# Kernel optimization log

Hardware: AMD Instinct MI355X
Metric: run time of the kernel (lower is better)

Reference implementation:

```python
import jax, jax.numpy as jnp
import numpy as np


def setup_inputs() -> dict:
    key = jax.random.key(0)
    k1, k2 = jax.random.split(key)
    z = jax.random.normal(k1, (16, 2048, 512), dtype=jnp.float32)
    embedding = jax.random.normal(k2, (8192, 512), dtype=jnp.float32)
    return {"z": z, "embedding": embedding}


def reference(z, embedding):
    BETA = 0.25
    B, N, D = z.shape
    n_codes = embedding.shape[0]
    flat_z = z.reshape(-1, D)  # [M, D], M = B*N
    # squared euclidean distances: ||z||^2 - 2 z.e^T + ||e||^2 -> [M, n_codes]
    dist = (jnp.sum(flat_z * flat_z, axis=1, keepdims=True)
            - 2.0 * jnp.matmul(flat_z, embedding.T)
            + jnp.sum(embedding * embedding, axis=1))
    codes = jnp.argmin(dist, axis=1)  # [M]
    z_q = embedding[codes].reshape(B, N, D)
    # straight-through estimator
    z_q_st = z + jax.lax.stop_gradient(z_q - z)
    loss = BETA * jnp.mean((z_q_st - jax.lax.stop_gradient(z)) ** 2)
    # codebook usage stats (equivalent to one_hot.mean(0))
    counts = jnp.zeros((n_codes,), dtype=flat_z.dtype).at[codes].add(1.0)
    avg_probs = counts / flat_z.shape[0]
    perp = jnp.exp(-jnp.sum(avg_probs * jnp.log(avg_probs + 1e-10)))
    return z_q_st, codes.reshape(B, N), loss, perp
```

## Files before the change

kernel.cpp:

```cpp
#include <hip/hip_runtime.h>
#include <stdint.h>
#include <stddef.h>

#define M_ROWS 32768
#define N_CODES 8192
#define K_DIM 512
#define BM 128
#define BN 128
#define BK 64
#define KITERS (K_DIM / BK)
#define CAND_CAP (3u*1024u*1024u)
#define LCAP 512u
#define TAU2 2.0f

#define OFF_CODES 16777216
#define OFF_LOSS  (16777216 + 32768)
#define OFF_PERP  (16777216 + 32768 + 1)

using short8  = __attribute__((ext_vector_type(8))) short;
using ushort8 = __attribute__((ext_vector_type(8))) unsigned short;
using f32x4   = __attribute__((ext_vector_type(4))) float;

typedef unsigned short u16;
typedef unsigned int   u32;
typedef unsigned long long u64;

__device__ __forceinline__ u32 ford(float f) {
    u32 u = __float_as_uint(f);
    return (u & 0x80000000u) ? ~u : (u | 0x80000000u);
}
__device__ __forceinline__ float fordinv(u32 u) {
    u32 v = (u & 0x80000000u) ? (u & 0x7FFFFFFFu) : ~u;
    return __uint_as_float(v);
}
__device__ __forceinline__ u16 f2bf(float f) {
    u32 u = __float_as_uint(f);
    u = u + 0x7FFFu + ((u >> 16) & 1u);
    return (u16)(u >> 16);
}

__device__ __forceinline__ void ldg_to_lds16(const u16* g, u16* l) {
    __builtin_amdgcn_global_load_lds((__attribute__((address_space(1))) void*)(g),
                                     (__attribute__((address_space(3))) void*)(l),
                                     16, 0, 0);
}

__global__ void k_init(u32* rowMin, u64* rowBest, u32* counts, u32* candCnt) {
    int i = blockIdx.x * blockDim.x + threadIdx.x;
    if (i < M_ROWS) { rowMin[i] = 0xFFFFFFFFu; rowBest[i] = ~0ull; }
    if (i < N_CODES) counts[i] = 0u;
    if (i == 0) *candCnt = 0u;
}

__global__ void k_convert(const float* __restrict__ src, u16* __restrict__ dst,
                          float* __restrict__ nrm2, int nrows) {
    int row  = blockIdx.x * 4 + (threadIdx.x >> 6);
    int lane = threadIdx.x & 63;
    if (row >= nrows) return;
    const float* p = src + (size_t)row * K_DIM + lane * 8;
    float4 a = *(const float4*)p;
    float4 b = *(const float4*)(p + 4);
    ushort8 v;
    v[0]=f2bf(a.x); v[1]=f2bf(a.y); v[2]=f2bf(a.z); v[3]=f2bf(a.w);
    v[4]=f2bf(b.x); v[5]=f2bf(b.y); v[6]=f2bf(b.z); v[7]=f2bf(b.w);
    *(ushort8*)(dst + (size_t)row * K_DIM + lane * 8) = v;
    float ss = a.x*a.x + a.y*a.y + a.z*a.z + a.w*a.w
             + b.x*b.x + b.y*b.y + b.z*b.z + b.w*b.w;
    #pragma unroll
    for (int s = 32; s; s >>= 1) ss += __shfl_xor(ss, s);
    if (lane == 0) nrm2[row] = ss;
}

__global__ __launch_bounds__(256, 4)
void k_gemm(const u16* __restrict__ zb, const u16* __restrict__ eb,
            const float* __restrict__ en2, u32* __restrict__ rowMin,
            u32* __restrict__ candCnt, u64* __restrict__ cand) {
    __shared__ __align__(16) u16 As[BM * BK];
    __shared__ __align__(16) u16 Bs[BN * BK];
    __shared__ float en2s[BN];
    __shared__ u32 threshL[BM];
    __shared__ u64 candBuf[LCAP];
    __shared__ u32 ldsCnt, ldsBase;

    const int tid  = threadIdx.x;
    const int lane = tid & 63;
    const int wave = tid >> 6;
    const int rowTile = blockIdx.x * BM;
    const int nTile   = blockIdx.y * BN;
    const int wm = (wave >> 1) * 64;
    const int wn = (wave & 1) * 64;

    if (tid < BN) { en2s[tid] = en2[nTile + tid]; threshL[tid] = 0xFFFFFFFFu; }
    if (tid == 0) ldsCnt = 0u;

    const int srow = (lane >> 3);
    const int sg   = (lane & 7) ^ ((lane >> 3) & 7);
    const u16* gA[4]; const u16* gB[4]; u16* lA[4]; u16* lB[4];
    #pragma unroll
    for (int t = 0; t < 4; t++) {
        int i = wave * 4 + t;
        gA[t] = zb + (size_t)(rowTile + i * 8 + srow) * K_DIM + sg * 8;
        gB[t] = eb + (size_t)(nTile   + i * 8 + srow) * K_DIM + sg * 8;
        lA[t] = As + i * 512;
        lB[t] = Bs + i * 512;
    }

    int aoff[4], boff[4];
    const int q = lane >> 4;
    #pragma unroll
    for (int t = 0; t < 4; t++) {
        int R  = wm + t * 16 + (lane & 15);
        aoff[t] = (R * 8 + (q ^ (R & 7))) * 16;
        int Rn = wn + t * 16 + (lane & 15);
        boff[t] = (Rn * 8 + (q ^ (Rn & 7))) * 16;
    }

    f32x4 acc[4][4] = {};

    for (int kk = 0; kk < KITERS; kk++) {
        const int ko = kk * BK;
        #pragma unroll
        for (int t = 0; t < 4; t++) {
            ldg_to_lds16(gA[t] + ko, lA[t]);
            ldg_to_lds16(gB[t] + ko, lB[t]);
        }
        __syncthreads();
        short8 af[4], bf_[4];
        #pragma unroll
        for (int t = 0; t < 4; t++) {
            af[t]  = *(const short8*)((const char*)As + aoff[t]);
            bf_[t] = *(const short8*)((const char*)Bs + boff[t]);
        }
        #pragma unroll
        for (int i = 0; i < 4; i++)
            #pragma unroll
            for (int j = 0; j < 4; j++)
                acc[i][j] = __builtin_amdgcn_mfma_f32_16x16x32_bf16(af[i], bf_[j], acc[i][j], 0, 0, 0);
        #pragma unroll
        for (int t = 0; t < 4; t++) {
            af[t]  = *(const short8*)((const char*)As + (aoff[t] ^ 64));
            bf_[t] = *(const short8*)((const char*)Bs + (boff[t] ^ 64));
        }
        #pragma unroll
        for (int i = 0; i < 4; i++)
            #pragma unroll
            for (int j = 0; j < 4; j++)
                acc[i][j] = __builtin_amdgcn_mfma_f32_16x16x32_bf16(af[i], bf_[j], acc[i][j], 0, 0, 0);
        __syncthreads();
    }

    float e2v[4];
    #pragma unroll
    for (int j = 0; j < 4; j++) e2v[j] = en2s[wn + j * 16 + (lane & 15)];
    #pragma unroll
    for (int i = 0; i < 4; i++)
        #pragma unroll
        for (int j = 0; j < 4; j++)
            #pragma unroll
            for (int r = 0; r < 4; r++)
                acc[i][j][r] = e2v[j] - 2.0f * acc[i][j][r];

    float rm[4][4];
    #pragma unroll
    for (int i = 0; i < 4; i++)
        #pragma unroll
        for (int r = 0; r < 4; r++)
            rm[i][r] = fminf(fminf(acc[i][0][r], acc[i][1][r]),
                             fminf(acc[i][2][r], acc[i][3][r]));
    #pragma unroll
    for (int d = 1; d < 16; d <<= 1)
        #pragma unroll
        for (int i = 0; i < 4; i++)
            #pragma unroll
            for (int r = 0; r < 4; r++)
                rm[i][r] = fminf(rm[i][r], __shfl_xor(rm[i][r], d));

    if ((lane & 15) == 0) {
        #pragma unroll
        for (int i = 0; i < 4; i++)
            #pragma unroll
            for (int r = 0; r < 4; r++) {
                int lrow = wm + i * 16 + (lane >> 4) * 4 + r;
                u32 o = ford(rm[i][r]);
                atomicMin(&threshL[lrow], o);
                u32 old = atomicMin(&rowMin[rowTile + lrow], o);
                atomicMin(&threshL[lrow], old);
            }
    }
    __syncthreads();

    #pragma unroll
    for (int i = 0; i < 4; i++) {
        #pragma unroll
        for (int r = 0; r < 4; r++) {
            int lrow = wm + i * 16 + (lane >> 4) * 4 + r;
            float th = fordinv(threshL[lrow]) + TAU2;
            #pragma unroll
            for (int j = 0; j < 4; j++) {
                float sv = acc[i][j][r];
                if (sv <= th) {
                    u32 code = (u32)(nTile + wn + j * 16 + (lane & 15));
                    u64 pk = ((u64)ford(sv) << 32) |
                             (u64)(((u32)(rowTile + lrow) << 13) | code);
                    u32 idx = atomicAdd(&ldsCnt, 1u);
                    if (idx < LCAP) candBuf[idx] = pk;
                    else { u32 g = atomicAdd(candCnt, 1u);
                           if (g < CAND_CAP) cand[g] = pk; }
                }
            }
        }
    }
    __syncthreads();
    if (tid == 0) {
        u32 n = ldsCnt < LCAP ? ldsCnt : LCAP;
        ldsBase = atomicAdd(candCnt, n);
    }
    __syncthreads();
    u32 n = ldsCnt < LCAP ? ldsCnt : LCAP;
    for (u32 k2 = tid; k2 < n; k2 += 256) {
        u32 g = ldsBase + k2;
        if (g < CAND_CAP) cand[g] = candBuf[k2];
    }
}

__global__ void k_refine(const float* __restrict__ z, const float* __restrict__ emb,
                         const float* __restrict__ en2, const u32* __restrict__ candCnt,
                         const u64* __restrict__ cand, const u32* __restrict__ rowMin,
                         u64* __restrict__ rowBest) {
    u32 cnt = *candCnt; if (cnt > CAND_CAP) cnt = CAND_CAP;
    int gt = blockIdx.x * blockDim.x + threadIdx.x;
    u32 wid = (u32)(gt >> 6);
    int lane = gt & 63;
    u32 nw = (u32)((gridDim.x * blockDim.x) >> 6);
    for (u32 ci = wid; ci < cnt; ci += nw) {
        u64 pk = cand[ci];
        u32 rc = (u32)pk;
        u32 row = rc >> 13, code = rc & (N_CODES - 1);
        float ad = fordinv((u32)(pk >> 32));
        float gm = fordinv(rowMin[row]);
        if (ad > gm + TAU2) continue;
        const float4* zp = (const float4*)(z + (size_t)row * K_DIM) + lane * 2;
        const float4* ep = (const float4*)(emb + (size_t)code * K_DIM) + lane * 2;
        float4 a0 = zp[0], a1 = zp[1], b0 = ep[0], b1 = ep[1];
        float d = a0.x*b0.x + a0.y*b0.y + a0.z*b0.z + a0.w*b0.w
                + a1.x*b1.x + a1.y*b1.y + a1.z*b1.z + a1.w*b1.w;
        #pragma unroll
        for (int s = 32; s; s >>= 1) d += __shfl_xor(d, s);
        if (lane == 0) {
            float sv = en2[code] - 2.0f * d;
            u64 bk = ((u64)ford(sv) << 32) | (u64)code;
            atomicMin(rowBest + row, bk);
        }
    }
}

__global__ void k_output(const u64* __restrict__ rowBest, const float* __restrict__ emb,
                         float* __restrict__ out, u32* __restrict__ counts) {
    int row = blockIdx.x;
    u64 pk = rowBest[row];
    u32 code = (u32)(pk & 0xFFFFFFFFull);
    int t = threadIdx.x;
    float4 v = ((const float4*)(emb + (size_t)code * K_DIM))[t];
    ((float4*)(out + (size_t)row * K_DIM))[t] = v;
    if (t == 0) {
        out[OFF_CODES + row] = (float)code;
        atomicAdd(&counts[code], 1u);
    }
}

__global__ void k_final(const u64* __restrict__ rowBest, const float* __restrict__ zn2,
                        const u32* __restrict__ counts, float* __restrict__ out) {
    __shared__ float red[256];
    int t = threadIdx.x;
    float s1 = 0.f;
    for (int r = t; r < M_ROWS; r += 256)
        s1 += zn2[r] + fordinv((u32)(rowBest[r] >> 32));
    red[t] = s1; __syncthreads();
    for (int w = 128; w; w >>= 1) { if (t < w) red[t] += red[t + w]; __syncthreads(); }
    float lossSum = red[0];
    __syncthreads();
    float s2 = 0.f;
    for (int c = t; c < N_CODES; c += 256) {
        float p = (float)counts[c] * (1.0f / (float)M_ROWS);
        s2 += p * logf(p + 1e-10f);
    }
    red[t] = s2; __syncthreads();
    for (int w = 128; w; w >>= 1) { if (t < w) red[t] += red[t + w]; __syncthreads(); }
    if (t == 0) {
        out[OFF_LOSS] = 0.25f * lossSum / ((float)M_ROWS * (float)K_DIM);
        out[OFF_PERP] = expf(-red[0]);
    }
}

#define WS_ZB      ((size_t)0)
#define WS_EB      ((size_t)33554432)
#define WS_EN2     ((size_t)41943040)
#define WS_ZN2     ((size_t)41975808)
#define WS_ROWMIN  ((size_t)42106880)
#define WS_ROWBEST ((size_t)42237952)
#define WS_COUNTS  ((size_t)42500096)
#define WS_CANDCNT ((size_t)42532864)
#define WS_CAND    ((size_t)42533120)

extern "C" void kernel_launch(void* const* d_in, const int* in_sizes, int n_in,
                              void* d_out, int out_size, void* d_ws, size_t ws_size,
                              hipStream_t stream) {
    const float* z   = (const float*)d_in[0];
    const float* emb = (const float*)d_in[1];
    float* out = (float*)d_out;
    char* ws = (char*)d_ws;

    u16*  zb      = (u16*)(ws + WS_ZB);
    u16*  eb      = (u16*)(ws + WS_EB);
    float* en2    = (float*)(ws + WS_EN2);
    float* zn2    = (float*)(ws + WS_ZN2);
    u32*  rowMin  = (u32*)(ws + WS_ROWMIN);
    u64*  rowBest = (u64*)(ws + WS_ROWBEST);
    u32*  counts  = (u32*)(ws + WS_COUNTS);
    u32*  candCnt = (u32*)(ws + WS_CANDCNT);
    u64*  cand    = (u64*)(ws + WS_CAND);

    k_init<<<dim3(M_ROWS / 256), dim3(256), 0, stream>>>(rowMin, rowBest, counts, candCnt);
    k_convert<<<dim3(M_ROWS / 4), dim3(256), 0, stream>>>(z, zb, zn2, M_ROWS);
    k_convert<<<dim3(N_CODES / 4), dim3(256), 0, stream>>>(emb, eb, en2, N_CODES);
    k_gemm<<<dim3(M_ROWS / BM, N_CODES / BN), dim3(256), 0, stream>>>(zb, eb, en2, rowMin, candCnt, cand);
    k_refine<<<dim3(1024), dim3(256), 0, stream>>>(z, emb, en2, candCnt, cand, rowMin, rowBest);
    k_output<<<dim3(M_ROWS), dim3(128), 0, stream>>>(rowBest, emb, out, counts);
    k_final<<<dim3(1), dim3(256), 0, stream>>>(rowBest, zn2, counts, out);
}
```

Measured before the change: 647.7 us.

## Fuse init into convert, batch refine candidates, widen output and parallelize final

```diff
diff --git a/kernel.cpp b/kernel.cpp
--- a/kernel.cpp
+++ b/kernel.cpp
@@ -45,15 +45,16 @@
                                      16, 0, 0);
 }
 
-__global__ void k_init(u32* rowMin, u64* rowBest, u32* counts, u32* candCnt) {
-    int i = blockIdx.x * blockDim.x + threadIdx.x;
-    if (i < M_ROWS) { rowMin[i] = 0xFFFFFFFFu; rowBest[i] = ~0ull; }
-    if (i < N_CODES) counts[i] = 0u;
-    if (i == 0) *candCnt = 0u;
-}
-
 __global__ void k_convert(const float* __restrict__ src, u16* __restrict__ dst,
-                          float* __restrict__ nrm2, int nrows) {
+                          float* __restrict__ nrm2, int nrows,
+                          u32* rowMin, u64* rowBest, u32* counts, u32* candCnt,
+                          float* fsum, u32* ticket) {
+    if (rowMin) {
+        int g = blockIdx.x * blockDim.x + threadIdx.x;
+        if (g < M_ROWS) { rowMin[g] = 0xFFFFFFFFu; rowBest[g] = ~0ull; }
+        if (g < N_CODES) counts[g] = 0u;
+        if (g == 0) { *candCnt = 0u; *fsum = 0.f; *ticket = 0u; }
+    }
     int row  = blockIdx.x * 4 + (threadIdx.x >> 6);
     int lane = threadIdx.x & 63;
     if (row >= nrows) return;
@@ -232,34 +233,46 @@
     u32 wid = (u32)(gt >> 6);
     int lane = gt & 63;
     u32 nw = (u32)((gridDim.x * blockDim.x) >> 6);
-    for (u32 ci = wid; ci < cnt; ci += nw) {
-        u64 pk = cand[ci];
-        u32 rc = (u32)pk;
-        u32 row = rc >> 13, code = rc & (N_CODES - 1);
-        float ad = fordinv((u32)(pk >> 32));
-        float gm = fordinv(rowMin[row]);
-        if (ad > gm + TAU2) continue;
-        const float4* zp = (const float4*)(z + (size_t)row * K_DIM) + lane * 2;
-        const float4* ep = (const float4*)(emb + (size_t)code * K_DIM) + lane * 2;
-        float4 a0 = zp[0], a1 = zp[1], b0 = ep[0], b1 = ep[1];
-        float d = a0.x*b0.x + a0.y*b0.y + a0.z*b0.z + a0.w*b0.w
-                + a1.x*b1.x + a1.y*b1.y + a1.z*b1.z + a1.w*b1.w;
-        #pragma unroll
-        for (int s = 32; s; s >>= 1) d += __shfl_xor(d, s);
-        if (lane == 0) {
-            float sv = en2[code] - 2.0f * d;
-            u64 bk = ((u64)ford(sv) << 32) | (u64)code;
-            atomicMin(rowBest + row, bk);
+    for (u32 base = wid * 64u; base < cnt; base += nw * 64u) {
+        u32 ci = base + (u32)lane;
+        u32 row = 0, code = 0;
+        bool live = false;
+        if (ci < cnt) {
+            u64 pk = cand[ci];
+            u32 rc = (u32)pk;
+            row = rc >> 13; code = rc & (N_CODES - 1);
+            float ad = fordinv((u32)(pk >> 32));
+            float gm = fordinv(rowMin[row]);
+            live = (ad <= gm + TAU2);
+        }
+        u64 mask = __ballot(live);
+        while (mask) {
+            int s = (int)(__ffsll((long long)mask) - 1);
+            mask &= mask - 1;
+            u32 srow  = __shfl(row,  s);
+            u32 scode = __shfl(code, s);
+            const float4* zp = (const float4*)(z + (size_t)srow * K_DIM) + lane * 2;
+            const float4* ep = (const float4*)(emb + (size_t)scode * K_DIM) + lane * 2;
+            float4 a0 = zp[0], a1 = zp[1], b0 = ep[0], b1 = ep[1];
+            float d = a0.x*b0.x + a0.y*b0.y + a0.z*b0.z + a0.w*b0.w
+                    + a1.x*b1.x + a1.y*b1.y + a1.z*b1.z + a1.w*b1.w;
+            #pragma unroll
+            for (int sh = 32; sh; sh >>= 1) d += __shfl_xor(d, sh);
+            if (lane == 0) {
+                float sv = en2[scode] - 2.0f * d;
+                u64 bk = ((u64)ford(sv) << 32) | (u64)scode;
+                atomicMin(rowBest + srow, bk);
+            }
         }
     }
 }
 
 __global__ void k_output(const u64* __restrict__ rowBest, const float* __restrict__ emb,
                          float* __restrict__ out, u32* __restrict__ counts) {
-    int row = blockIdx.x;
+    int row = blockIdx.x * 4 + (threadIdx.x >> 7);
+    int t   = threadIdx.x & 127;
     u64 pk = rowBest[row];
     u32 code = (u32)(pk & 0xFFFFFFFFull);
-    int t = threadIdx.x;
     float4 v = ((const float4*)(emb + (size_t)code * K_DIM))[t];
     ((float4*)(out + (size_t)row * K_DIM))[t] = v;
     if (t == 0) {
@@ -269,16 +282,25 @@
 }
 
 __global__ void k_final(const u64* __restrict__ rowBest, const float* __restrict__ zn2,
-                        const u32* __restrict__ counts, float* __restrict__ out) {
+                        const u32* __restrict__ counts, float* __restrict__ out,
+                        float* __restrict__ fsum, u32* __restrict__ ticket) {
     __shared__ float red[256];
+    __shared__ int lastBlk;
+    __shared__ float lossSumSh;
     int t = threadIdx.x;
     float s1 = 0.f;
-    for (int r = t; r < M_ROWS; r += 256)
+    for (int r = blockIdx.x * 256 + t; r < M_ROWS; r += gridDim.x * 256)
         s1 += zn2[r] + fordinv((u32)(rowBest[r] >> 32));
     red[t] = s1; __syncthreads();
     for (int w = 128; w; w >>= 1) { if (t < w) red[t] += red[t + w]; __syncthreads(); }
-    float lossSum = red[0];
+    if (t == 0) {
+        atomicAdd(fsum, red[0]);
+        __threadfence();
+        lastBlk = (atomicAdd(ticket, 1u) == gridDim.x - 1) ? 1 : 0;
+    }
     __syncthreads();
+    if (!lastBlk) return;
+    if (t == 0) lossSumSh = atomicAdd(fsum, 0.0f);
     float s2 = 0.f;
     for (int c = t; c < N_CODES; c += 256) {
         float p = (float)counts[c] * (1.0f / (float)M_ROWS);
@@ -287,7 +309,7 @@
     red[t] = s2; __syncthreads();
     for (int w = 128; w; w >>= 1) { if (t < w) red[t] += red[t + w]; __syncthreads(); }
     if (t == 0) {
-        out[OFF_LOSS] = 0.25f * lossSum / ((float)M_ROWS * (float)K_DIM);
+        out[OFF_LOSS] = 0.25f * lossSumSh / ((float)M_ROWS * (float)K_DIM);
         out[OFF_PERP] = expf(-red[0]);
     }
 }
@@ -318,13 +340,16 @@
     u64*  rowBest = (u64*)(ws + WS_ROWBEST);
     u32*  counts  = (u32*)(ws + WS_COUNTS);
     u32*  candCnt = (u32*)(ws + WS_CANDCNT);
+    float* fsum   = (float*)(ws + WS_CANDCNT + 8);
+    u32*  ticket  = (u32*)(ws + WS_CANDCNT + 12);
     u64*  cand    = (u64*)(ws + WS_CAND);
 
-    k_init<<<dim3(M_ROWS / 256), dim3(256), 0, stream>>>(rowMin, rowBest, counts, candCnt);
-    k_convert<<<dim3(M_ROWS / 4), dim3(256), 0, stream>>>(z, zb, zn2, M_ROWS);
-    k_convert<<<dim3(N_CODES / 4), dim3(256), 0, stream>>>(emb, eb, en2, N_CODES);
+    k_convert<<<dim3(M_ROWS / 4), dim3(256), 0, stream>>>(z, zb, zn2, M_ROWS,
+                                                          rowMin, rowBest, counts, candCnt, fsum, ticket);
+    k_convert<<<dim3(N_CODES / 4), dim3(256), 0, stream>>>(emb, eb, en2, N_CODES,
+                                                           nullptr, nullptr, nullptr, nullptr, nullptr, nullptr);
     k_gemm<<<dim3(M_ROWS / BM, N_CODES / BN), dim3(256), 0, stream>>>(zb, eb, en2, rowMin, candCnt, cand);
     k_refine<<<dim3(1024), dim3(256), 0, stream>>>(z, emb, en2, candCnt, cand, rowMin, rowBest);
-    k_output<<<dim3(M_ROWS), dim3(128), 0, stream>>>(rowBest, emb, out, counts);
-    k_final<<<dim3(1), dim3(256), 0, stream>>>(rowBest, zn2, counts, out);
-}
+    k_output<<<dim3(M_ROWS / 4), dim3(512), 0, stream>>>(rowBest, emb, out, counts);
+    k_final<<<dim3(32), dim3(256), 0, stream>>>(rowBest, zn2, counts, out, fsum, ticket);
+}
```

Measured after the change: 627.8 us (median of 2 runs). -3.1%, faster.
